# Kernel tuning notes

Measured on AMD Instinct MI355X. Metric: run time of the kernel, lower is better.

## Reference

```python
import jax, jax.numpy as jnp
import numpy as np

N_NODES = 100000
N_EDGES = 3200000
D_IN = 256
D_HID = 256
N_CLASS = 40


def setup_inputs() -> dict:
    key = jax.random.key(0)
    ks = jax.random.split(key, 8)
    x = jax.random.normal(ks[0], (N_NODES, D_IN), dtype=jnp.float32)
    edge_index = jax.random.randint(ks[1], (2, N_EDGES), 0, N_NODES, dtype=jnp.int64)
    s1 = 1.0 / np.sqrt(D_IN)
    s2 = 1.0 / np.sqrt(D_HID)
    W1_l = jax.random.normal(ks[2], (D_IN, D_HID), dtype=jnp.float32) * s1
    W1_r = jax.random.normal(ks[3], (D_IN, D_HID), dtype=jnp.float32) * s1
    b1 = jnp.zeros((D_HID,), dtype=jnp.float32)
    W2_l = jax.random.normal(ks[4], (D_HID, N_CLASS), dtype=jnp.float32) * s2
    W2_r = jax.random.normal(ks[5], (D_HID, N_CLASS), dtype=jnp.float32) * s2
    b2 = jnp.zeros((N_CLASS,), dtype=jnp.float32)
    return {"x": x, "edge_index": edge_index, "W1_l": W1_l, "W1_r": W1_r,
            "b1": b1, "W2_l": W2_l, "W2_r": W2_r, "b2": b2}


def _sage_conv(h, src, dst, deg_inv, Wl, Wr, b):
    # mean-aggregate source features into targets, then linear transforms
    agg = jax.ops.segment_sum(h[src], dst, num_segments=N_NODES)  # [N, d]
    agg = agg * deg_inv[:, None]
    return agg @ Wl + h @ Wr + b


def reference(x, edge_index, W1_l, W1_r, b1, W2_l, W2_r, b2):
    src, dst = edge_index[0], edge_index[1]
    deg = jax.ops.segment_sum(jnp.ones((src.shape[0],), dtype=x.dtype), dst,
                              num_segments=N_NODES)
    deg_inv = 1.0 / jnp.maximum(deg, 1.0)
    h = jax.nn.relu(_sage_conv(x, src, dst, deg_inv, W1_l, W1_r, b1))
    out = _sage_conv(h, src, dst, deg_inv, W2_l, W2_r, b2)
    return jax.nn.log_softmax(out, axis=1)
```

## Files before the change

kernel.cpp:

```cpp
#include <hip/hip_runtime.h>
#include <hip/hip_bf16.h>

#define THREADS 256
#define NB_MAX 400
#define NPH 13

typedef __attribute__((ext_vector_type(8))) short bf16x8;
typedef __attribute__((ext_vector_type(4))) float f32x4;
typedef __attribute__((ext_vector_type(2))) float f32x2;

__device__ __forceinline__ unsigned short f2b(float f) {
    __hip_bfloat16 h = __float2bfloat16(f);
    return *reinterpret_cast<unsigned short*>(&h);
}
__device__ __forceinline__ unsigned char f2q(float v) {
    int q = __builtin_amdgcn_cvt_pk_fp8_f32(v, v, 0, false);
    return (unsigned char)(q & 0xff);
}
__device__ __forceinline__ void gload_lds16(const void* g, void* l) {
    __builtin_amdgcn_global_load_lds(
        (const __attribute__((address_space(1))) void*)g,
        (__attribute__((address_space(3))) void*)l, 16, 0, 0);
}

__global__ __launch_bounds__(256) void k_hist(const int* __restrict__ dst, int E, int nbk,
                                              int* __restrict__ gcnt) {
    __shared__ int lc[NB_MAX];
    const int tid = threadIdx.x;
    for (int i = tid; i < nbk; i += 256) lc[i] = 0;
    __syncthreads();
    const int stride = gridDim.x * 256;
    for (int e = blockIdx.x * 256 + tid; e < E; e += stride)
        atomicAdd(&lc[dst[e] >> 8], 1);
    __syncthreads();
    for (int i = tid; i < nbk; i += 256)
        if (lc[i]) atomicAdd(&gcnt[i], lc[i]);
}

__global__ __launch_bounds__(512) void k_scanb(const int* __restrict__ gcnt, int* __restrict__ bptr,
                                               int* __restrict__ gcur, int nbk, int E) {
    __shared__ int sm[512];
    const int t = threadIdx.x;
    int v = (t < nbk) ? gcnt[t] : 0;
    sm[t] = v; __syncthreads();
    for (int off = 1; off < 512; off <<= 1) {
        int u = (t >= off) ? sm[t - off] : 0; __syncthreads();
        sm[t] += u; __syncthreads();
    }
    if (t < nbk) {
        int ex = sm[t] - v;
        bptr[t] = ex;
        gcur[t] = ex;
    }
    if (t == 0) bptr[nbk] = E;
}

__global__ __launch_bounds__(256) void k_bucket_scatter(const int* __restrict__ src, const int* __restrict__ dst,
                                                        int* __restrict__ gcur, unsigned* __restrict__ pairs,
                                                        int E, int nbk) {
    __shared__ int cnt[NB_MAX];
    __shared__ int base[NB_MAX];
    const int tid = threadIdx.x;
    const int e0 = blockIdx.x * 8192;
    for (int i = tid; i < nbk; i += 256) cnt[i] = 0;
    __syncthreads();
    #pragma unroll
    for (int j = 0; j < 32; ++j) {
        int e = e0 + j * 256 + tid;
        if (e < E) atomicAdd(&cnt[dst[e] >> 8], 1);
    }
    __syncthreads();
    for (int i = tid; i < nbk; i += 256)
        base[i] = cnt[i] ? atomicAdd(&gcur[i], cnt[i]) : 0;
    __syncthreads();
    #pragma unroll
    for (int j = 0; j < 32; ++j) {
        int e = e0 + j * 256 + tid;
        if (e < E) {
            int d = dst[e];
            int p = atomicAdd(&base[d >> 8], 1);
            pairs[p] = ((unsigned)src[e] << 8) | ((unsigned)d & 255u);
        }
    }
}

__global__ __launch_bounds__(256) void k_bucket_csr(const int* __restrict__ bptr, const unsigned* __restrict__ pairs,
                                                    int* __restrict__ rowptr, float* __restrict__ dinv,
                                                    int* __restrict__ csr_src, int N, int nbk, int E) {
    __shared__ int pc[256 * NPH];
    __shared__ int deg[256];
    __shared__ int sm[256];
    __shared__ int nodebase[256];
    const int b = blockIdx.x;
    const int tid = threadIdx.x;
    const int e0 = bptr[b], e1 = bptr[b + 1];

    #pragma unroll
    for (int i = 0; i < NPH; ++i) pc[i * 256 + tid] = 0;
    __syncthreads();
    for (int e = e0 + tid; e < e1; e += 256) {
        unsigned u = pairs[e];
        int n = (int)(u & 255u);
        int ph = (int)(u >> 8) >> 13;
        atomicAdd(&pc[ph * 256 + n], 1);
    }
    __syncthreads();
    int run = 0;
    #pragma unroll
    for (int ph = 0; ph < NPH; ++ph) {
        int c = pc[ph * 256 + tid];
        pc[ph * 256 + tid] = run;
        run += c;
    }
    int d = run;
    deg[tid] = d;
    sm[tid] = d; __syncthreads();
    for (int off = 1; off < 256; off <<= 1) {
        int u = (tid >= off) ? sm[tid - off] : 0; __syncthreads();
        sm[tid] += u; __syncthreads();
    }
    int ex = sm[tid] - d;
    int node = (b << 8) + tid;
    int nb_ = e0 + ex;
    nodebase[tid] = nb_;
    if (node < N) {
        rowptr[node] = nb_;
        dinv[node] = 1.0f / (float)max(d, 1);
    }
    if (b == nbk - 1 && tid == 0) rowptr[N] = E;
    __syncthreads();
    #pragma unroll
    for (int ph = 0; ph < NPH; ++ph) pc[ph * 256 + tid] += nodebase[tid];
    __syncthreads();
    for (int e = e0 + tid; e < e1; e += 256) {
        unsigned u = pairs[e];
        int n = (int)(u & 255u);
        int s = (int)(u >> 8);
        int p = atomicAdd(&pc[(s >> 13) * 256 + n], 1);
        csr_src[p] = s;
    }
}

__global__ __launch_bounds__(256) void k_cvt(const float* __restrict__ x, unsigned short* __restrict__ xb,
                                             unsigned char* __restrict__ xq, int N, int Npad,
                                             const float* __restrict__ W1l, const float* __restrict__ W1r,
                                             const float* __restrict__ W2l, const float* __restrict__ W2r,
                                             unsigned short* __restrict__ WbT, unsigned short* __restrict__ WbT2) {
    int i = blockIdx.x * THREADS + threadIdx.x;
    const int nxu = Npad * 32;
    if (i < nxu) {
        int row = i >> 5;
        unsigned short o[8];
        int q0 = 0, q1 = 0;
        if (row < N) {
            float4 v0 = reinterpret_cast<const float4*>(x)[2 * (size_t)i];
            float4 v1 = reinterpret_cast<const float4*>(x)[2 * (size_t)i + 1];
            o[0] = f2b(v0.x); o[1] = f2b(v0.y); o[2] = f2b(v0.z); o[3] = f2b(v0.w);
            o[4] = f2b(v1.x); o[5] = f2b(v1.y); o[6] = f2b(v1.z); o[7] = f2b(v1.w);
            q0 = __builtin_amdgcn_cvt_pk_fp8_f32(v0.x, v0.y, q0, false);
            q0 = __builtin_amdgcn_cvt_pk_fp8_f32(v0.z, v0.w, q0, true);
            q1 = __builtin_amdgcn_cvt_pk_fp8_f32(v1.x, v1.y, q1, false);
            q1 = __builtin_amdgcn_cvt_pk_fp8_f32(v1.z, v1.w, q1, true);
        } else {
            #pragma unroll
            for (int j = 0; j < 8; ++j) o[j] = 0;
        }
        reinterpret_cast<uint4*>(xb)[i] = *reinterpret_cast<uint4*>(o);
        reinterpret_cast<uint2*>(xq)[i] = make_uint2((unsigned)q0, (unsigned)q1);
        return;
    }
    int idx = i - nxu;
    if (idx < 131072) {
        int n = idx >> 9, k = idx & 511;
        float v = (k < 256) ? W1l[(size_t)k * 256 + n] : W1r[(size_t)(k - 256) * 256 + n];
        WbT[idx] = f2b(v);
    } else if (idx < 131072 + 20480) {
        int j = idx - 131072;
        int n = j >> 8, k = j & 255;
        float v = (n < 40) ? W2l[(size_t)k * 40 + n] : W2r[(size_t)k * 40 + (n - 40)];
        WbT2[j] = f2b(v);
    }
}

__global__ __launch_bounds__(256) void k_agg1(const int* __restrict__ rowptr, const int* __restrict__ csr_src,
                                              const float* __restrict__ dinv, const unsigned char* __restrict__ xq,
                                              unsigned short* __restrict__ aggb, int N, int Npad) {
    int gid = blockIdx.x * THREADS + threadIdx.x;
    int node = gid >> 5, lane = gid & 31;
    if (node >= N) {
        if (node < Npad)
            reinterpret_cast<uint4*>(aggb + (size_t)node * 256 + lane * 8)[0] = make_uint4(0, 0, 0, 0);
        return;
    }
    const int e0 = rowptr[node], e1 = rowptr[node + 1];
    const unsigned char* xl = xq + (size_t)lane * 8;
    f32x2 acc[4];
    #pragma unroll
    for (int j = 0; j < 4; ++j) acc[j] = (f32x2){0.f, 0.f};
    for (int eb = e0; eb < e1; eb += 32) {
        int n = min(32, e1 - eb);
        int sidx = (eb + lane < e1) ? csr_src[eb + lane] : 0;
        int j = 0;
        for (; j + 7 < n; j += 8) {
            uint2 vv[8];
            #pragma unroll
            for (int q = 0; q < 8; ++q) {
                int s = __shfl(sidx, j + q, 32);
                vv[q] = *reinterpret_cast<const uint2*>(xl + (size_t)s * 256);
            }
            #pragma unroll
            for (int q = 0; q < 8; ++q) {
                acc[0] += __builtin_amdgcn_cvt_pk_f32_fp8((int)vv[q].x, false);
                acc[1] += __builtin_amdgcn_cvt_pk_f32_fp8((int)vv[q].x, true);
                acc[2] += __builtin_amdgcn_cvt_pk_f32_fp8((int)vv[q].y, false);
                acc[3] += __builtin_amdgcn_cvt_pk_f32_fp8((int)vv[q].y, true);
            }
        }
        for (; j < n; ++j) {
            int s = __shfl(sidx, j, 32);
            uint2 v = *reinterpret_cast<const uint2*>(xl + (size_t)s * 256);
            acc[0] += __builtin_amdgcn_cvt_pk_f32_fp8((int)v.x, false);
            acc[1] += __builtin_amdgcn_cvt_pk_f32_fp8((int)v.x, true);
            acc[2] += __builtin_amdgcn_cvt_pk_f32_fp8((int)v.y, false);
            acc[3] += __builtin_amdgcn_cvt_pk_f32_fp8((int)v.y, true);
        }
    }
    const float ds = dinv[node];
    unsigned short o[8];
    #pragma unroll
    for (int j = 0; j < 4; ++j) {
        o[2 * j + 0] = f2b(acc[j].x * ds);
        o[2 * j + 1] = f2b(acc[j].y * ds);
    }
    *reinterpret_cast<uint4*>(aggb + (size_t)node * 256 + lane * 8) = *reinterpret_cast<uint4*>(o);
}

__global__ __launch_bounds__(512) void k_gemm1(
    const unsigned short* __restrict__ aggb, const unsigned short* __restrict__ xb,
    const unsigned short* __restrict__ WbT, const float* __restrict__ b1,
    unsigned short* __restrict__ hb, int M)
{
    __shared__ unsigned short As[128 * 64];
    __shared__ unsigned short Bs[256 * 64];

    const int tid  = threadIdx.x;
    const int lane = tid & 63;
    const int wave = tid >> 6;
    const int row0 = blockIdx.x * 128;
    const int wm0  = (wave >> 2) * 64;
    const int wn0  = (wave & 3) * 64;

    const int ldr = lane >> 3;
    const int lsw = ((lane & 7) ^ ldr) * 8;

    f32x4 acc[4][4];
    #pragma unroll
    for (int m = 0; m < 4; ++m)
        #pragma unroll
        for (int n = 0; n < 4; ++n)
            acc[m][n] = (f32x4){0.f, 0.f, 0.f, 0.f};

    for (int kt = 0; kt < 8; ++kt) {
        const unsigned short* Abase = (kt < 4) ? aggb : xb;
        const int kcol = (kt & 3) * 64;
        __syncthreads();
        #pragma unroll
        for (int i = 0; i < 2; ++i) {
            const int c = wave * 2 + i;
            const unsigned short* ga = Abase + (size_t)(row0 + c * 8 + ldr) * 256 + kcol + lsw;
            gload_lds16(ga, &As[c * 512]);
        }
        #pragma unroll
        for (int i = 0; i < 4; ++i) {
            const int c = wave * 4 + i;
            const unsigned short* gb = WbT + (size_t)(c * 8 + ldr) * 512 + kt * 64 + lsw;
            gload_lds16(gb, &Bs[c * 512]);
        }
        __syncthreads();
        #pragma unroll
        for (int kk = 0; kk < 2; ++kk) {
            bf16x8 af[4], bf[4];
            #pragma unroll
            for (int m = 0; m < 4; ++m) {
                const int r = wm0 + m * 16 + (lane & 15);
                const int s = (kk * 4 + (lane >> 4)) ^ (r & 7);
                af[m] = *reinterpret_cast<const bf16x8*>(&As[r * 64 + s * 8]);
            }
            #pragma unroll
            for (int n = 0; n < 4; ++n) {
                const int r = wn0 + n * 16 + (lane & 15);
                const int s = (kk * 4 + (lane >> 4)) ^ (r & 7);
                bf[n] = *reinterpret_cast<const bf16x8*>(&Bs[r * 64 + s * 8]);
            }
            #pragma unroll
            for (int m = 0; m < 4; ++m)
                #pragma unroll
                for (int n = 0; n < 4; ++n)
                    acc[m][n] = __builtin_amdgcn_mfma_f32_16x16x32_bf16(af[m], bf[n], acc[m][n], 0, 0, 0);
        }
    }

    const int crow = (lane >> 4) * 4;
    const int ccol = lane & 15;
    #pragma unroll
    for (int n = 0; n < 4; ++n) {
        const int col = wn0 + n * 16 + ccol;
        const float bias = b1[col];
        #pragma unroll
        for (int m = 0; m < 4; ++m) {
            const int rbase = row0 + wm0 + m * 16 + crow;
            #pragma unroll
            for (int r = 0; r < 4; ++r) {
                const int row = rbase + r;
                if (row < M) {
                    float v = fmaxf(acc[m][n][r] + bias, 0.f);
                    hb[(size_t)row * 256 + col] = f2b(v);
                }
            }
        }
    }
}

__global__ __launch_bounds__(256) void k_gemm2(
    const unsigned short* __restrict__ hb, const unsigned short* __restrict__ WbT2,
    const float* __restrict__ b2,
    unsigned char* __restrict__ Tq, float* __restrict__ Up, int M)
{
    __shared__ unsigned short As[128 * 64];
    __shared__ unsigned short Bs2[80 * 264];

    const int tid  = threadIdx.x;
    const int lane = tid & 63;
    const int wave = tid >> 6;
    const int row0 = blockIdx.x * 128;

    const int ldr = lane >> 3;
    const int lsw = ((lane & 7) ^ ldr) * 8;

    for (int idx = tid; idx < 80 * 32; idx += 256) {
        int row = idx >> 5, un = idx & 31;
        uint4 d = *reinterpret_cast<const uint4*>(WbT2 + (size_t)row * 256 + un * 8);
        *reinterpret_cast<uint4*>(&Bs2[row * 264 + un * 8]) = d;
    }

    f32x4 acc[2][5];
    #pragma unroll
    for (int m = 0; m < 2; ++m)
        #pragma unroll
        for (int n = 0; n < 5; ++n)
            acc[m][n] = (f32x4){0.f, 0.f, 0.f, 0.f};

    for (int kt = 0; kt < 4; ++kt) {
        __syncthreads();
        #pragma unroll
        for (int i = 0; i < 4; ++i) {
            const int c = wave * 4 + i;
            const unsigned short* ga = hb + (size_t)(row0 + c * 8 + ldr) * 256 + kt * 64 + lsw;
            gload_lds16(ga, &As[c * 512]);
        }
        __syncthreads();
        #pragma unroll
        for (int kk = 0; kk < 2; ++kk) {
            bf16x8 af[2], bf[5];
            #pragma unroll
            for (int m = 0; m < 2; ++m) {
                const int r = wave * 32 + m * 16 + (lane & 15);
                const int s = (kk * 4 + (lane >> 4)) ^ (r & 7);
                af[m] = *reinterpret_cast<const bf16x8*>(&As[(r & 127) * 64 + s * 8]);
            }
            #pragma unroll
            for (int n = 0; n < 5; ++n) {
                const int r = n * 16 + (lane & 15);
                bf[n] = *reinterpret_cast<const bf16x8*>(&Bs2[r * 264 + kt * 64 + kk * 32 + (lane >> 4) * 8]);
            }
            #pragma unroll
            for (int m = 0; m < 2; ++m)
                #pragma unroll
                for (int n = 0; n < 5; ++n)
                    acc[m][n] = __builtin_amdgcn_mfma_f32_16x16x32_bf16(af[m], bf[n], acc[m][n], 0, 0, 0);
        }
    }

    const int crow = (lane >> 4) * 4;
    const int ccol = lane & 15;
    #pragma unroll
    for (int n = 0; n < 5; ++n) {
        const int col = n * 16 + ccol;
        #pragma unroll
        for (int m = 0; m < 2; ++m) {
            const int rbase = row0 + wave * 32 + m * 16 + crow;
            #pragma unroll
            for (int r = 0; r < 4; ++r) {
                const int row = rbase + r;
                if (row < M) {
                    float v = acc[m][n][r];
                    if (col < 40)
                        Tq[(size_t)row * 40 + col] = f2q(v);
                    else
                        Up[(size_t)row * 40 + (col - 40)] = v + b2[col - 40];
                }
            }
        }
    }
}

__global__ __launch_bounds__(256) void k_final(const int* __restrict__ rowptr, const int* __restrict__ csr_src,
                                               const float* __restrict__ dinv, const unsigned char* __restrict__ Tq,
                                               const float* __restrict__ Up, float* __restrict__ out, int N) {
    int gid = blockIdx.x * THREADS + threadIdx.x;
    int node = gid >> 6, lane = gid & 63;
    if (node >= N) return;
    const int e0 = rowptr[node], e1 = rowptr[node + 1];
    const int g = lane / 10;
    const int c = lane % 10;
    float a0 = 0.f, a1 = 0.f, a2 = 0.f, a3 = 0.f;
    for (int eb = e0; eb < e1; eb += 64) {
        int sidx = (eb + lane < e1) ? csr_src[eb + lane] : 0;
        int nn = min(64, e1 - eb);
        for (int jb = 0; jb < nn; jb += 6) {
            int ei = jb + g;
            bool valid = (g < 6) && (ei < nn);
            int s = __shfl(sidx, ei & 63, 64);
            if (valid) {
                unsigned u = *reinterpret_cast<const unsigned*>(Tq + (size_t)s * 40 + c * 4);
                f32x2 lo = __builtin_amdgcn_cvt_pk_f32_fp8((int)u, false);
                f32x2 hi = __builtin_amdgcn_cvt_pk_f32_fp8((int)u, true);
                a0 += lo.x; a1 += lo.y;
                a2 += hi.x; a3 += hi.y;
            }
        }
    }
    float t0 = a0, t1 = a1, t2 = a2, t3 = a3;
    #pragma unroll
    for (int gg = 1; gg < 6; ++gg) {
        t0 += __shfl(a0, c + 10 * gg, 64);
        t1 += __shfl(a1, c + 10 * gg, 64);
        t2 += __shfl(a2, c + 10 * gg, 64);
        t3 += __shfl(a3, c + 10 * gg, 64);
    }
    float v0 = -1e30f, v1 = -1e30f, v2 = -1e30f, v3 = -1e30f;
    if (lane < 10) {
        const float ds = dinv[node];
        float4 up = *reinterpret_cast<const float4*>(Up + (size_t)node * 40 + lane * 4);
        v0 = t0 * ds + up.x; v1 = t1 * ds + up.y;
        v2 = t2 * ds + up.z; v3 = t3 * ds + up.w;
    }
    float m = fmaxf(fmaxf(v0, v1), fmaxf(v2, v3));
    #pragma unroll
    for (int o = 8; o > 0; o >>= 1) m = fmaxf(m, __shfl_xor(m, o, 16));
    float e = 0.f;
    if (lane < 10) e = expf(v0 - m) + expf(v1 - m) + expf(v2 - m) + expf(v3 - m);
    float ssum = e;
    #pragma unroll
    for (int o = 8; o > 0; o >>= 1) ssum += __shfl_xor(ssum, o, 16);
    float ls = logf(ssum);
    if (lane < 10) {
        float4 o4;
        o4.x = v0 - m - ls; o4.y = v1 - m - ls;
        o4.z = v2 - m - ls; o4.w = v3 - m - ls;
        *reinterpret_cast<float4*>(out + (size_t)node * 40 + lane * 4) = o4;
    }
}

extern "C" void kernel_launch(void* const* d_in, const int* in_sizes, int n_in,
                              void* d_out, int out_size, void* d_ws, size_t ws_size,
                              hipStream_t stream) {
    const float* x   = (const float*)d_in[0];
    const int*   ei  = (const int*)d_in[1];
    const float* W1l = (const float*)d_in[2];
    const float* W1r = (const float*)d_in[3];
    const float* b1  = (const float*)d_in[4];
    const float* W2l = (const float*)d_in[5];
    const float* W2r = (const float*)d_in[6];
    const float* b2  = (const float*)d_in[7];
    float* out = (float*)d_out;

    const int N = in_sizes[0] / 256;
    const int E = in_sizes[1] / 2;
    const int Npad = ((N + 127) / 128) * 128;
    const int nbk = (N + 255) / 256;
    const int* src = ei;
    const int* dst = ei + E;

    char* ws = (char*)d_ws;
    size_t off = 0;
    int*   gcnt    = (int*)(ws + off); off += (size_t)NB_MAX * 4;
    int*   bptr    = (int*)(ws + off); off += (size_t)(NB_MAX + 1) * 4;
    int*   gcur    = (int*)(ws + off); off += (size_t)NB_MAX * 4;
    int*   rowptr  = (int*)(ws + off); off += (size_t)(N + 1) * 4;
    float* dinv    = (float*)(ws + off); off += (size_t)N * 4;
    off = (off + 255) & ~(size_t)255;
    unsigned* pairs = (unsigned*)(ws + off); off += (size_t)E * 4;
    int*   csr_src = (int*)(ws + off); off += (size_t)E * 4;
    off = (off + 255) & ~(size_t)255;
    unsigned short* xb   = (unsigned short*)(ws + off); off += (size_t)Npad * 256 * 2;
    unsigned char*  xq   = (unsigned char*)(ws + off);  off += (size_t)Npad * 256;
    unsigned short* aggb = (unsigned short*)(ws + off); off += (size_t)Npad * 256 * 2;
    unsigned short* hb   = (unsigned short*)(ws + off); off += (size_t)Npad * 256 * 2;
    unsigned short* WbT  = (unsigned short*)(ws + off); off += (size_t)256 * 512 * 2;
    unsigned short* WbT2 = (unsigned short*)(ws + off); off += (size_t)80 * 256 * 2;
    off = (off + 255) & ~(size_t)255;
    unsigned char*  Tq   = (unsigned char*)(ws + off);  off += (size_t)Npad * 40;
    off = (off + 255) & ~(size_t)255;
    float*          Up   = (float*)(ws + off);          off += (size_t)Npad * 40 * 4;

    hipMemsetAsync(gcnt, 0, (size_t)NB_MAX * 4, stream);

    const int nsb = (E + 8191) / 8192;
    k_hist<<<nsb, THREADS, 0, stream>>>(dst, E, nbk, gcnt);
    k_scanb<<<1, 512, 0, stream>>>(gcnt, bptr, gcur, nbk, E);
    k_bucket_scatter<<<nsb, THREADS, 0, stream>>>(src, dst, gcur, pairs, E, nbk);
    k_bucket_csr<<<nbk, THREADS, 0, stream>>>(bptr, pairs, rowptr, dinv, csr_src, N, nbk, E);

    const int ncvt = Npad * 32 + 131072 + 20480;
    k_cvt<<<(ncvt + THREADS - 1) / THREADS, THREADS, 0, stream>>>(x, xb, xq, N, Npad,
                                                                  W1l, W1r, W2l, W2r, WbT, WbT2);

    k_agg1<<<((size_t)Npad * 32 + THREADS - 1) / THREADS, THREADS, 0, stream>>>(rowptr, csr_src, dinv, xq, aggb, N, Npad);

    k_gemm1<<<Npad / 128, 512, 0, stream>>>(aggb, xb, WbT, b1, hb, N);

    k_gemm2<<<Npad / 128, THREADS, 0, stream>>>(hb, WbT2, b2, Tq, Up, N);

    k_final<<<((size_t)N * 64 + THREADS - 1) / THREADS, THREADS, 0, stream>>>(rowptr, csr_src, dinv, Tq, Up, out, N);
}
```

Measured before the change: 401.4 us.

## Phase-synchronized aggregation over source-range phases and fuse histogram with conversion

The first-layer aggregation now runs as a persistent grid. Each half-wave owns 13 nodes and walks the 13 source-ID phases in lockstep, with a block barrier between phases. The aim is for all blocks to gather from the same slice of the fp8 feature table at once, so that slice stays in L2. The CSR build also writes per-phase row pointers, and the edge histogram is merged with the feature and weight conversion into one launch. In exchange the kernel holds 13 accumulator sets in registers, which may spill or cut occupancy, the 8-wide unrolled gather loop is dropped, and load balance across nodes gets worse.

```diff
diff --git a/kernel.cpp b/kernel.cpp
--- a/kernel.cpp
+++ b/kernel.cpp
@@ -4,6 +4,8 @@
 #define THREADS 256
 #define NB_MAX 400
 #define NPH 13
+#define NB_AGG 1024
+#define OWN 13
 
 typedef __attribute__((ext_vector_type(8))) short bf16x8;
 typedef __attribute__((ext_vector_type(4))) float f32x4;
@@ -23,130 +25,27 @@
         (__attribute__((address_space(3))) void*)l, 16, 0, 0);
 }
 
-__global__ __launch_bounds__(256) void k_hist(const int* __restrict__ dst, int E, int nbk,
-                                              int* __restrict__ gcnt) {
+__global__ __launch_bounds__(256) void k_hist_cvt(
+    const int* __restrict__ dst, int E, int nbk, int* __restrict__ gcnt, int nsb,
+    const float* __restrict__ x, unsigned short* __restrict__ xb, unsigned char* __restrict__ xq,
+    int N, int Npad,
+    const float* __restrict__ W1l, const float* __restrict__ W1r,
+    const float* __restrict__ W2l, const float* __restrict__ W2r,
+    unsigned short* __restrict__ WbT, unsigned short* __restrict__ WbT2) {
     __shared__ int lc[NB_MAX];
     const int tid = threadIdx.x;
-    for (int i = tid; i < nbk; i += 256) lc[i] = 0;
-    __syncthreads();
-    const int stride = gridDim.x * 256;
-    for (int e = blockIdx.x * 256 + tid; e < E; e += stride)
-        atomicAdd(&lc[dst[e] >> 8], 1);
-    __syncthreads();
-    for (int i = tid; i < nbk; i += 256)
-        if (lc[i]) atomicAdd(&gcnt[i], lc[i]);
-}
-
-__global__ __launch_bounds__(512) void k_scanb(const int* __restrict__ gcnt, int* __restrict__ bptr,
-                                               int* __restrict__ gcur, int nbk, int E) {
-    __shared__ int sm[512];
-    const int t = threadIdx.x;
-    int v = (t < nbk) ? gcnt[t] : 0;
-    sm[t] = v; __syncthreads();
-    for (int off = 1; off < 512; off <<= 1) {
-        int u = (t >= off) ? sm[t - off] : 0; __syncthreads();
-        sm[t] += u; __syncthreads();
-    }
-    if (t < nbk) {
-        int ex = sm[t] - v;
-        bptr[t] = ex;
-        gcur[t] = ex;
-    }
-    if (t == 0) bptr[nbk] = E;
-}
-
-__global__ __launch_bounds__(256) void k_bucket_scatter(const int* __restrict__ src, const int* __restrict__ dst,
-                                                        int* __restrict__ gcur, unsigned* __restrict__ pairs,
-                                                        int E, int nbk) {
-    __shared__ int cnt[NB_MAX];
-    __shared__ int base[NB_MAX];
-    const int tid = threadIdx.x;
-    const int e0 = blockIdx.x * 8192;
-    for (int i = tid; i < nbk; i += 256) cnt[i] = 0;
-    __syncthreads();
-    #pragma unroll
-    for (int j = 0; j < 32; ++j) {
-        int e = e0 + j * 256 + tid;
-        if (e < E) atomicAdd(&cnt[dst[e] >> 8], 1);
-    }
-    __syncthreads();
-    for (int i = tid; i < nbk; i += 256)
-        base[i] = cnt[i] ? atomicAdd(&gcur[i], cnt[i]) : 0;
-    __syncthreads();
-    #pragma unroll
-    for (int j = 0; j < 32; ++j) {
-        int e = e0 + j * 256 + tid;
-        if (e < E) {
-            int d = dst[e];
-            int p = atomicAdd(&base[d >> 8], 1);
-            pairs[p] = ((unsigned)src[e] << 8) | ((unsigned)d & 255u);
-        }
-    }
-}
-
-__global__ __launch_bounds__(256) void k_bucket_csr(const int* __restrict__ bptr, const unsigned* __restrict__ pairs,
-                                                    int* __restrict__ rowptr, float* __restrict__ dinv,
-                                                    int* __restrict__ csr_src, int N, int nbk, int E) {
-    __shared__ int pc[256 * NPH];
-    __shared__ int deg[256];
-    __shared__ int sm[256];
-    __shared__ int nodebase[256];
-    const int b = blockIdx.x;
-    const int tid = threadIdx.x;
-    const int e0 = bptr[b], e1 = bptr[b + 1];
-
-    #pragma unroll
-    for (int i = 0; i < NPH; ++i) pc[i * 256 + tid] = 0;
-    __syncthreads();
-    for (int e = e0 + tid; e < e1; e += 256) {
-        unsigned u = pairs[e];
-        int n = (int)(u & 255u);
-        int ph = (int)(u >> 8) >> 13;
-        atomicAdd(&pc[ph * 256 + n], 1);
-    }
-    __syncthreads();
-    int run = 0;
-    #pragma unroll
-    for (int ph = 0; ph < NPH; ++ph) {
-        int c = pc[ph * 256 + tid];
-        pc[ph * 256 + tid] = run;
-        run += c;
-    }
-    int d = run;
-    deg[tid] = d;
-    sm[tid] = d; __syncthreads();
-    for (int off = 1; off < 256; off <<= 1) {
-        int u = (tid >= off) ? sm[tid - off] : 0; __syncthreads();
-        sm[tid] += u; __syncthreads();
-    }
-    int ex = sm[tid] - d;
-    int node = (b << 8) + tid;
-    int nb_ = e0 + ex;
-    nodebase[tid] = nb_;
-    if (node < N) {
-        rowptr[node] = nb_;
-        dinv[node] = 1.0f / (float)max(d, 1);
-    }
-    if (b == nbk - 1 && tid == 0) rowptr[N] = E;
-    __syncthreads();
-    #pragma unroll
-    for (int ph = 0; ph < NPH; ++ph) pc[ph * 256 + tid] += nodebase[tid];
-    __syncthreads();
-    for (int e = e0 + tid; e < e1; e += 256) {
-        unsigned u = pairs[e];
-        int n = (int)(u & 255u);
-        int s = (int)(u >> 8);
-        int p = atomicAdd(&pc[(s >> 13) * 256 + n], 1);
-        csr_src[p] = s;
-    }
-}
-
-__global__ __launch_bounds__(256) void k_cvt(const float* __restrict__ x, unsigned short* __restrict__ xb,
-                                             unsigned char* __restrict__ xq, int N, int Npad,
-                                             const float* __restrict__ W1l, const float* __restrict__ W1r,
-                                             const float* __restrict__ W2l, const float* __restrict__ W2r,
-                                             unsigned short* __restrict__ WbT, unsigned short* __restrict__ WbT2) {
-    int i = blockIdx.x * THREADS + threadIdx.x;
+    if ((int)blockIdx.x < nsb) {
+        for (int i = tid; i < nbk; i += 256) lc[i] = 0;
+        __syncthreads();
+        const int stride = nsb * 256;
+        for (int e = blockIdx.x * 256 + tid; e < E; e += stride)
+            atomicAdd(&lc[dst[e] >> 8], 1);
+        __syncthreads();
+        for (int i = tid; i < nbk; i += 256)
+            if (lc[i]) atomicAdd(&gcnt[i], lc[i]);
+        return;
+    }
+    int i = ((int)blockIdx.x - nsb) * 256 + tid;
     const int nxu = Npad * 32;
     if (i < nxu) {
         int row = i >> 5;
@@ -182,57 +81,169 @@
     }
 }
 
-__global__ __launch_bounds__(256) void k_agg1(const int* __restrict__ rowptr, const int* __restrict__ csr_src,
+__global__ __launch_bounds__(512) void k_scanb(const int* __restrict__ gcnt, int* __restrict__ bptr,
+                                               int* __restrict__ gcur, int nbk, int E) {
+    __shared__ int sm[512];
+    const int t = threadIdx.x;
+    int v = (t < nbk) ? gcnt[t] : 0;
+    sm[t] = v; __syncthreads();
+    for (int off = 1; off < 512; off <<= 1) {
+        int u = (t >= off) ? sm[t - off] : 0; __syncthreads();
+        sm[t] += u; __syncthreads();
+    }
+    if (t < nbk) {
+        int ex = sm[t] - v;
+        bptr[t] = ex;
+        gcur[t] = ex;
+    }
+    if (t == 0) bptr[nbk] = E;
+}
+
+__global__ __launch_bounds__(256) void k_bucket_scatter(const int* __restrict__ src, const int* __restrict__ dst,
+                                                        int* __restrict__ gcur, unsigned* __restrict__ pairs,
+                                                        int E, int nbk) {
+    __shared__ int cnt[NB_MAX];
+    __shared__ int base[NB_MAX];
+    const int tid = threadIdx.x;
+    const int e0 = blockIdx.x * 8192;
+    for (int i = tid; i < nbk; i += 256) cnt[i] = 0;
+    __syncthreads();
+    #pragma unroll
+    for (int j = 0; j < 32; ++j) {
+        int e = e0 + j * 256 + tid;
+        if (e < E) atomicAdd(&cnt[dst[e] >> 8], 1);
+    }
+    __syncthreads();
+    for (int i = tid; i < nbk; i += 256)
+        base[i] = cnt[i] ? atomicAdd(&gcur[i], cnt[i]) : 0;
+    __syncthreads();
+    #pragma unroll
+    for (int j = 0; j < 32; ++j) {
+        int e = e0 + j * 256 + tid;
+        if (e < E) {
+            int d = dst[e];
+            int p = atomicAdd(&base[d >> 8], 1);
+            pairs[p] = ((unsigned)src[e] << 8) | ((unsigned)d & 255u);
+        }
+    }
+}
+
+__global__ __launch_bounds__(256) void k_bucket_csr(const int* __restrict__ bptr, const unsigned* __restrict__ pairs,
+                                                    int* __restrict__ rowptr, int* __restrict__ rowptr2,
+                                                    float* __restrict__ dinv,
+                                                    int* __restrict__ csr_src, int N, int nbk, int E) {
+    __shared__ int pc[256 * NPH];
+    __shared__ int deg[256];
+    __shared__ int sm[256];
+    __shared__ int nodebase[256];
+    const int b = blockIdx.x;
+    const int tid = threadIdx.x;
+    const int e0 = bptr[b], e1 = bptr[b + 1];
+
+    #pragma unroll
+    for (int i = 0; i < NPH; ++i) pc[i * 256 + tid] = 0;
+    __syncthreads();
+    for (int e = e0 + tid; e < e1; e += 256) {
+        unsigned u = pairs[e];
+        int n = (int)(u & 255u);
+        int ph = (int)(u >> 8) >> 13;
+        atomicAdd(&pc[ph * 256 + n], 1);
+    }
+    __syncthreads();
+    int run = 0;
+    #pragma unroll
+    for (int ph = 0; ph < NPH; ++ph) {
+        int c = pc[ph * 256 + tid];
+        pc[ph * 256 + tid] = run;
+        run += c;
+    }
+    int d = run;
+    deg[tid] = d;
+    sm[tid] = d; __syncthreads();
+    for (int off = 1; off < 256; off <<= 1) {
+        int u = (tid >= off) ? sm[tid - off] : 0; __syncthreads();
+        sm[tid] += u; __syncthreads();
+    }
+    int ex = sm[tid] - d;
+    int node = (b << 8) + tid;
+    int nb_ = e0 + ex;
+    nodebase[tid] = nb_;
+    if (node < N) {
+        rowptr[node] = nb_;
+        dinv[node] = 1.0f / (float)max(d, 1);
+    }
+    if (b == nbk - 1 && tid == 0) rowptr[N] = E;
+    __syncthreads();
+    #pragma unroll
+    for (int ph = 0; ph < NPH; ++ph) {
+        int cu = pc[ph * 256 + tid] + nodebase[tid];
+        pc[ph * 256 + tid] = cu;
+        if (node < N) rowptr2[(size_t)ph * N + node] = cu;
+    }
+    if (node < N) rowptr2[(size_t)NPH * N + node] = nb_ + d;
+    __syncthreads();
+    for (int e = e0 + tid; e < e1; e += 256) {
+        unsigned u = pairs[e];
+        int n = (int)(u & 255u);
+        int s = (int)(u >> 8);
+        int p = atomicAdd(&pc[(s >> 13) * 256 + n], 1);
+        csr_src[p] = s;
+    }
+}
+
+__global__ __launch_bounds__(256) void k_agg1(const int* __restrict__ rowptr2, const int* __restrict__ csr_src,
                                               const float* __restrict__ dinv, const unsigned char* __restrict__ xq,
-                                              unsigned short* __restrict__ aggb, int N, int Npad) {
-    int gid = blockIdx.x * THREADS + threadIdx.x;
-    int node = gid >> 5, lane = gid & 31;
-    if (node >= N) {
-        if (node < Npad)
-            reinterpret_cast<uint4*>(aggb + (size_t)node * 256 + lane * 8)[0] = make_uint4(0, 0, 0, 0);
-        return;
-    }
-    const int e0 = rowptr[node], e1 = rowptr[node + 1];
+                                              unsigned short* __restrict__ aggb, int N, int Npad, int H) {
+    const int tid = threadIdx.x;
+    const int hw = blockIdx.x * 8 + (tid >> 5);
+    const int lane = tid & 31;
     const unsigned char* xl = xq + (size_t)lane * 8;
-    f32x2 acc[4];
-    #pragma unroll
-    for (int j = 0; j < 4; ++j) acc[j] = (f32x2){0.f, 0.f};
-    for (int eb = e0; eb < e1; eb += 32) {
-        int n = min(32, e1 - eb);
-        int sidx = (eb + lane < e1) ? csr_src[eb + lane] : 0;
-        int j = 0;
-        for (; j + 7 < n; j += 8) {
-            uint2 vv[8];
-            #pragma unroll
-            for (int q = 0; q < 8; ++q) {
-                int s = __shfl(sidx, j + q, 32);
-                vv[q] = *reinterpret_cast<const uint2*>(xl + (size_t)s * 256);
-            }
-            #pragma unroll
-            for (int q = 0; q < 8; ++q) {
-                acc[0] += __builtin_amdgcn_cvt_pk_f32_fp8((int)vv[q].x, false);
-                acc[1] += __builtin_amdgcn_cvt_pk_f32_fp8((int)vv[q].x, true);
-                acc[2] += __builtin_amdgcn_cvt_pk_f32_fp8((int)vv[q].y, false);
-                acc[3] += __builtin_amdgcn_cvt_pk_f32_fp8((int)vv[q].y, true);
-            }
-        }
-        for (; j < n; ++j) {
-            int s = __shfl(sidx, j, 32);
-            uint2 v = *reinterpret_cast<const uint2*>(xl + (size_t)s * 256);
-            acc[0] += __builtin_amdgcn_cvt_pk_f32_fp8((int)v.x, false);
-            acc[1] += __builtin_amdgcn_cvt_pk_f32_fp8((int)v.x, true);
-            acc[2] += __builtin_amdgcn_cvt_pk_f32_fp8((int)v.y, false);
-            acc[3] += __builtin_amdgcn_cvt_pk_f32_fp8((int)v.y, true);
-        }
-    }
-    const float ds = dinv[node];
-    unsigned short o[8];
-    #pragma unroll
-    for (int j = 0; j < 4; ++j) {
-        o[2 * j + 0] = f2b(acc[j].x * ds);
-        o[2 * j + 1] = f2b(acc[j].y * ds);
-    }
-    *reinterpret_cast<uint4*>(aggb + (size_t)node * 256 + lane * 8) = *reinterpret_cast<uint4*>(o);
+
+    f32x2 acc[OWN][4];
+    #pragma unroll
+    for (int i = 0; i < OWN; ++i)
+        #pragma unroll
+        for (int j = 0; j < 4; ++j) acc[i][j] = (f32x2){0.f, 0.f};
+
+    for (int ph = 0; ph < NPH; ++ph) {
+        #pragma unroll
+        for (int i = 0; i < OWN; ++i) {
+            const int node = hw + i * H;
+            if (node >= N) continue;
+            const int s0 = rowptr2[(size_t)ph * N + node];
+            const int s1 = rowptr2[(size_t)(ph + 1) * N + node];
+            for (int eb = s0; eb < s1; eb += 32) {
+                int cnt = min(32, s1 - eb);
+                int sidx = (eb + lane < s1) ? csr_src[eb + lane] : 0;
+                for (int j = 0; j < cnt; ++j) {
+                    int s = __shfl(sidx, j, 32);
+                    uint2 v = *reinterpret_cast<const uint2*>(xl + (size_t)s * 256);
+                    acc[i][0] += __builtin_amdgcn_cvt_pk_f32_fp8((int)v.x, false);
+                    acc[i][1] += __builtin_amdgcn_cvt_pk_f32_fp8((int)v.x, true);
+                    acc[i][2] += __builtin_amdgcn_cvt_pk_f32_fp8((int)v.y, false);
+                    acc[i][3] += __builtin_amdgcn_cvt_pk_f32_fp8((int)v.y, true);
+                }
+            }
+        }
+        __syncthreads();
+    }
+
+    #pragma unroll
+    for (int i = 0; i < OWN; ++i) {
+        const int node = hw + i * H;
+        if (node < N) {
+            const float ds = dinv[node];
+            unsigned short o[8];
+            #pragma unroll
+            for (int j = 0; j < 4; ++j) {
+                o[2 * j + 0] = f2b(acc[i][j].x * ds);
+                o[2 * j + 1] = f2b(acc[i][j].y * ds);
+            }
+            *reinterpret_cast<uint4*>(aggb + (size_t)node * 256 + lane * 8) = *reinterpret_cast<uint4*>(o);
+        } else if (node < Npad) {
+            *reinterpret_cast<uint4*>(aggb + (size_t)node * 256 + lane * 8) = make_uint4(0, 0, 0, 0);
+        }
+    }
 }
 
 __global__ __launch_bounds__(512) void k_gemm1(
@@ -490,6 +501,8 @@
     int*   rowptr  = (int*)(ws + off); off += (size_t)(N + 1) * 4;
     float* dinv    = (float*)(ws + off); off += (size_t)N * 4;
     off = (off + 255) & ~(size_t)255;
+    int*   rowptr2 = (int*)(ws + off); off += (size_t)(NPH + 1) * N * 4;
+    off = (off + 255) & ~(size_t)255;
     unsigned* pairs = (unsigned*)(ws + off); off += (size_t)E * 4;
     int*   csr_src = (int*)(ws + off); off += (size_t)E * 4;
     off = (off + 255) & ~(size_t)255;
@@ -507,16 +520,16 @@
     hipMemsetAsync(gcnt, 0, (size_t)NB_MAX * 4, stream);
 
     const int nsb = (E + 8191) / 8192;
-    k_hist<<<nsb, THREADS, 0, stream>>>(dst, E, nbk, gcnt);
+    const int ncvt_blocks = (Npad * 32 + 131072 + 20480 + THREADS - 1) / THREADS;
+    k_hist_cvt<<<nsb + ncvt_blocks, THREADS, 0, stream>>>(dst, E, nbk, gcnt, nsb,
+                                                          x, xb, xq, N, Npad,
+                                                          W1l, W1r, W2l, W2r, WbT, WbT2);
     k_scanb<<<1, 512, 0, stream>>>(gcnt, bptr, gcur, nbk, E);
     k_bucket_scatter<<<nsb, THREADS, 0, stream>>>(src, dst, gcur, pairs, E, nbk);
-    k_bucket_csr<<<nbk, THREADS, 0, stream>>>(bptr, pairs, rowptr, dinv, csr_src, N, nbk, E);
-
-    const int ncvt = Npad * 32 + 131072 + 20480;
-    k_cvt<<<(ncvt + THREADS - 1) / THREADS, THREADS, 0, stream>>>(x, xb, xq, N, Npad,
-                                                                  W1l, W1r, W2l, W2r, WbT, WbT2);
-
-    k_agg1<<<((size_t)Npad * 32 + THREADS - 1) / THREADS, THREADS, 0, stream>>>(rowptr, csr_src, dinv, xq, aggb, N, Npad);
+    k_bucket_csr<<<nbk, THREADS, 0, stream>>>(bptr, pairs, rowptr, rowptr2, dinv, csr_src, N, nbk, E);
+
+    const int H = NB_AGG * 8;
+    k_agg1<<<NB_AGG, THREADS, 0, stream>>>(rowptr2, csr_src, dinv, xq, aggb, N, Npad, H);
 
     k_gemm1<<<Npad / 128, 512, 0, stream>>>(aggb, xb, WbT, b1, hb, N);
 
```

Measured after the change: 848.0 us. 111% more time.

## Fuse histogram with conversion kernel and pad FP8 logits rows to 64 bytes

Applied to the files above, without the earlier changes.

The edge-destination histogram and the x/weight conversion now run as one launch, with blocks split by index, so the conversion overlaps the histogram and one launch is saved. The FP8 layer-2 projection buffer is padded from 40 to 64 bytes per row with zeroed padding. This lets the final gather kernel have 8 lanes read 8 bytes each per edge, processing 8 edges per step instead of 6 with a tree reduction. The trade-off is more gather bytes per edge plus extra padding writes in gemm2.

```diff
diff --git a/kernel.cpp b/kernel.cpp
--- a/kernel.cpp
+++ b/kernel.cpp
@@ -23,130 +23,27 @@
         (__attribute__((address_space(3))) void*)l, 16, 0, 0);
 }
 
-__global__ __launch_bounds__(256) void k_hist(const int* __restrict__ dst, int E, int nbk,
-                                              int* __restrict__ gcnt) {
+__global__ __launch_bounds__(256) void k_hist_cvt(
+    const int* __restrict__ dst, int E, int nbk, int* __restrict__ gcnt, int nsb,
+    const float* __restrict__ x, unsigned short* __restrict__ xb, unsigned char* __restrict__ xq,
+    int N, int Npad,
+    const float* __restrict__ W1l, const float* __restrict__ W1r,
+    const float* __restrict__ W2l, const float* __restrict__ W2r,
+    unsigned short* __restrict__ WbT, unsigned short* __restrict__ WbT2) {
     __shared__ int lc[NB_MAX];
     const int tid = threadIdx.x;
-    for (int i = tid; i < nbk; i += 256) lc[i] = 0;
-    __syncthreads();
-    const int stride = gridDim.x * 256;
-    for (int e = blockIdx.x * 256 + tid; e < E; e += stride)
-        atomicAdd(&lc[dst[e] >> 8], 1);
-    __syncthreads();
-    for (int i = tid; i < nbk; i += 256)
-        if (lc[i]) atomicAdd(&gcnt[i], lc[i]);
-}
-
-__global__ __launch_bounds__(512) void k_scanb(const int* __restrict__ gcnt, int* __restrict__ bptr,
-                                               int* __restrict__ gcur, int nbk, int E) {
-    __shared__ int sm[512];
-    const int t = threadIdx.x;
-    int v = (t < nbk) ? gcnt[t] : 0;
-    sm[t] = v; __syncthreads();
-    for (int off = 1; off < 512; off <<= 1) {
-        int u = (t >= off) ? sm[t - off] : 0; __syncthreads();
-        sm[t] += u; __syncthreads();
-    }
-    if (t < nbk) {
-        int ex = sm[t] - v;
-        bptr[t] = ex;
-        gcur[t] = ex;
-    }
-    if (t == 0) bptr[nbk] = E;
-}
-
-__global__ __launch_bounds__(256) void k_bucket_scatter(const int* __restrict__ src, const int* __restrict__ dst,
-                                                        int* __restrict__ gcur, unsigned* __restrict__ pairs,
-                                                        int E, int nbk) {
-    __shared__ int cnt[NB_MAX];
-    __shared__ int base[NB_MAX];
-    const int tid = threadIdx.x;
-    const int e0 = blockIdx.x * 8192;
-    for (int i = tid; i < nbk; i += 256) cnt[i] = 0;
-    __syncthreads();
-    #pragma unroll
-    for (int j = 0; j < 32; ++j) {
-        int e = e0 + j * 256 + tid;
-        if (e < E) atomicAdd(&cnt[dst[e] >> 8], 1);
-    }
-    __syncthreads();
-    for (int i = tid; i < nbk; i += 256)
-        base[i] = cnt[i] ? atomicAdd(&gcur[i], cnt[i]) : 0;
-    __syncthreads();
-    #pragma unroll
-    for (int j = 0; j < 32; ++j) {
-        int e = e0 + j * 256 + tid;
-        if (e < E) {
-            int d = dst[e];
-            int p = atomicAdd(&base[d >> 8], 1);
-            pairs[p] = ((unsigned)src[e] << 8) | ((unsigned)d & 255u);
-        }
-    }
-}
-
-__global__ __launch_bounds__(256) void k_bucket_csr(const int* __restrict__ bptr, const unsigned* __restrict__ pairs,
-                                                    int* __restrict__ rowptr, float* __restrict__ dinv,
-                                                    int* __restrict__ csr_src, int N, int nbk, int E) {
-    __shared__ int pc[256 * NPH];
-    __shared__ int deg[256];
-    __shared__ int sm[256];
-    __shared__ int nodebase[256];
-    const int b = blockIdx.x;
-    const int tid = threadIdx.x;
-    const int e0 = bptr[b], e1 = bptr[b + 1];
-
-    #pragma unroll
-    for (int i = 0; i < NPH; ++i) pc[i * 256 + tid] = 0;
-    __syncthreads();
-    for (int e = e0 + tid; e < e1; e += 256) {
-        unsigned u = pairs[e];
-        int n = (int)(u & 255u);
-        int ph = (int)(u >> 8) >> 13;
-        atomicAdd(&pc[ph * 256 + n], 1);
-    }
-    __syncthreads();
-    int run = 0;
-    #pragma unroll
-    for (int ph = 0; ph < NPH; ++ph) {
-        int c = pc[ph * 256 + tid];
-        pc[ph * 256 + tid] = run;
-        run += c;
-    }
-    int d = run;
-    deg[tid] = d;
-    sm[tid] = d; __syncthreads();
-    for (int off = 1; off < 256; off <<= 1) {
-        int u = (tid >= off) ? sm[tid - off] : 0; __syncthreads();
-        sm[tid] += u; __syncthreads();
-    }
-    int ex = sm[tid] - d;
-    int node = (b << 8) + tid;
-    int nb_ = e0 + ex;
-    nodebase[tid] = nb_;
-    if (node < N) {
-        rowptr[node] = nb_;
-        dinv[node] = 1.0f / (float)max(d, 1);
-    }
-    if (b == nbk - 1 && tid == 0) rowptr[N] = E;
-    __syncthreads();
-    #pragma unroll
-    for (int ph = 0; ph < NPH; ++ph) pc[ph * 256 + tid] += nodebase[tid];
-    __syncthreads();
-    for (int e = e0 + tid; e < e1; e += 256) {
-        unsigned u = pairs[e];
-        int n = (int)(u & 255u);
-        int s = (int)(u >> 8);
-        int p = atomicAdd(&pc[(s >> 13) * 256 + n], 1);
-        csr_src[p] = s;
-    }
-}
-
-__global__ __launch_bounds__(256) void k_cvt(const float* __restrict__ x, unsigned short* __restrict__ xb,
-                                             unsigned char* __restrict__ xq, int N, int Npad,
-                                             const float* __restrict__ W1l, const float* __restrict__ W1r,
-                                             const float* __restrict__ W2l, const float* __restrict__ W2r,
-                                             unsigned short* __restrict__ WbT, unsigned short* __restrict__ WbT2) {
-    int i = blockIdx.x * THREADS + threadIdx.x;
+    if ((int)blockIdx.x < nsb) {
+        for (int i = tid; i < nbk; i += 256) lc[i] = 0;
+        __syncthreads();
+        const int stride = nsb * 256;
+        for (int e = blockIdx.x * 256 + tid; e < E; e += stride)
+            atomicAdd(&lc[dst[e] >> 8], 1);
+        __syncthreads();
+        for (int i = tid; i < nbk; i += 256)
+            if (lc[i]) atomicAdd(&gcnt[i], lc[i]);
+        return;
+    }
+    int i = ((int)blockIdx.x - nsb) * 256 + tid;
     const int nxu = Npad * 32;
     if (i < nxu) {
         int row = i >> 5;
@@ -182,6 +79,108 @@
     }
 }
 
+__global__ __launch_bounds__(512) void k_scanb(const int* __restrict__ gcnt, int* __restrict__ bptr,
+                                               int* __restrict__ gcur, int nbk, int E) {
+    __shared__ int sm[512];
+    const int t = threadIdx.x;
+    int v = (t < nbk) ? gcnt[t] : 0;
+    sm[t] = v; __syncthreads();
+    for (int off = 1; off < 512; off <<= 1) {
+        int u = (t >= off) ? sm[t - off] : 0; __syncthreads();
+        sm[t] += u; __syncthreads();
+    }
+    if (t < nbk) {
+        int ex = sm[t] - v;
+        bptr[t] = ex;
+        gcur[t] = ex;
+    }
+    if (t == 0) bptr[nbk] = E;
+}
+
+__global__ __launch_bounds__(256) void k_bucket_scatter(const int* __restrict__ src, const int* __restrict__ dst,
+                                                        int* __restrict__ gcur, unsigned* __restrict__ pairs,
+                                                        int E, int nbk) {
+    __shared__ int cnt[NB_MAX];
+    __shared__ int base[NB_MAX];
+    const int tid = threadIdx.x;
+    const int e0 = blockIdx.x * 8192;
+    for (int i = tid; i < nbk; i += 256) cnt[i] = 0;
+    __syncthreads();
+    #pragma unroll
+    for (int j = 0; j < 32; ++j) {
+        int e = e0 + j * 256 + tid;
+        if (e < E) atomicAdd(&cnt[dst[e] >> 8], 1);
+    }
+    __syncthreads();
+    for (int i = tid; i < nbk; i += 256)
+        base[i] = cnt[i] ? atomicAdd(&gcur[i], cnt[i]) : 0;
+    __syncthreads();
+    #pragma unroll
+    for (int j = 0; j < 32; ++j) {
+        int e = e0 + j * 256 + tid;
+        if (e < E) {
+            int d = dst[e];
+            int p = atomicAdd(&base[d >> 8], 1);
+            pairs[p] = ((unsigned)src[e] << 8) | ((unsigned)d & 255u);
+        }
+    }
+}
+
+__global__ __launch_bounds__(256) void k_bucket_csr(const int* __restrict__ bptr, const unsigned* __restrict__ pairs,
+                                                    int* __restrict__ rowptr, float* __restrict__ dinv,
+                                                    int* __restrict__ csr_src, int N, int nbk, int E) {
+    __shared__ int pc[256 * NPH];
+    __shared__ int sm[256];
+    __shared__ int nodebase[256];
+    const int b = blockIdx.x;
+    const int tid = threadIdx.x;
+    const int e0 = bptr[b], e1 = bptr[b + 1];
+
+    #pragma unroll
+    for (int i = 0; i < NPH; ++i) pc[i * 256 + tid] = 0;
+    __syncthreads();
+    for (int e = e0 + tid; e < e1; e += 256) {
+        unsigned u = pairs[e];
+        int n = (int)(u & 255u);
+        int ph = (int)(u >> 8) >> 13;
+        atomicAdd(&pc[ph * 256 + n], 1);
+    }
+    __syncthreads();
+    int run = 0;
+    #pragma unroll
+    for (int ph = 0; ph < NPH; ++ph) {
+        int c = pc[ph * 256 + tid];
+        pc[ph * 256 + tid] = run;
+        run += c;
+    }
+    int d = run;
+    sm[tid] = d; __syncthreads();
+    for (int off = 1; off < 256; off <<= 1) {
+        int u = (tid >= off) ? sm[tid - off] : 0; __syncthreads();
+        sm[tid] += u; __syncthreads();
+    }
+    int ex = sm[tid] - d;
+    int node = (b << 8) + tid;
+    int nb_ = e0 + ex;
+    nodebase[tid] = nb_;
+    if (node < N) {
+        rowptr[node] = nb_;
+        dinv[node] = 1.0f / (float)max(d, 1);
+    }
+    if (b == nbk - 1 && tid == 0) rowptr[N] = E;
+    __syncthreads();
+    #pragma unroll
+    for (int ph = 0; ph < NPH; ++ph) pc[ph * 256 + tid] += nodebase[tid];
+    __syncthreads();
+    for (int e = e0 + tid; e < e1; e += 256) {
+        unsigned u = pairs[e];
+        int n = (int)(u & 255u);
+        int s = (int)(u >> 8);
+        int p = atomicAdd(&pc[(s >> 13) * 256 + n], 1);
+        csr_src[p] = s;
+    }
+}
+
 __global__ __launch_bounds__(256) void k_agg1(const int* __restrict__ rowptr, const int* __restrict__ csr_src,
                                               const float* __restrict__ dinv, const unsigned char* __restrict__ xq,
                                               unsigned short* __restrict__ aggb, int N, int Npad) {
@@ -395,12 +394,17 @@
                 if (row < M) {
                     float v = acc[m][n][r];
                     if (col < 40)
-                        Tq[(size_t)row * 40 + col] = f2q(v);
+                        Tq[(size_t)row * 64 + col] = f2q(v);
                     else
                         Up[(size_t)row * 40 + (col - 40)] = v + b2[col - 40];
                 }
             }
         }
+    }
+    for (int i = tid; i < 128 * 24; i += 256) {
+        int r = i / 24, c = 40 + (i % 24);
+        int row = row0 + r;
+        if (row < M) Tq[(size_t)row * 64 + c] = 0;
     }
 }
 
@@ -411,54 +415,64 @@
     int node = gid >> 6, lane = gid & 63;
     if (node >= N) return;
     const int e0 = rowptr[node], e1 = rowptr[node + 1];
-    const int g = lane / 10;
-    const int c = lane % 10;
-    float a0 = 0.f, a1 = 0.f, a2 = 0.f, a3 = 0.f;
+    const int c8 = lane & 7;
+    const int e5 = lane >> 3;
+    f32x2 acc[4];
+    #pragma unroll
+    for (int i = 0; i < 4; ++i) acc[i] = (f32x2){0.f, 0.f};
     for (int eb = e0; eb < e1; eb += 64) {
         int sidx = (eb + lane < e1) ? csr_src[eb + lane] : 0;
         int nn = min(64, e1 - eb);
-        for (int jb = 0; jb < nn; jb += 6) {
-            int ei = jb + g;
-            bool valid = (g < 6) && (ei < nn);
+        for (int jb = 0; jb < nn; jb += 8) {
+            int ei = jb + e5;
             int s = __shfl(sidx, ei & 63, 64);
-            if (valid) {
-                unsigned u = *reinterpret_cast<const unsigned*>(Tq + (size_t)s * 40 + c * 4);
-                f32x2 lo = __builtin_amdgcn_cvt_pk_f32_fp8((int)u, false);
-                f32x2 hi = __builtin_amdgcn_cvt_pk_f32_fp8((int)u, true);
-                a0 += lo.x; a1 += lo.y;
-                a2 += hi.x; a3 += hi.y;
-            }
-        }
-    }
-    float t0 = a0, t1 = a1, t2 = a2, t3 = a3;
-    #pragma unroll
-    for (int gg = 1; gg < 6; ++gg) {
-        t0 += __shfl(a0, c + 10 * gg, 64);
-        t1 += __shfl(a1, c + 10 * gg, 64);
-        t2 += __shfl(a2, c + 10 * gg, 64);
-        t3 += __shfl(a3, c + 10 * gg, 64);
-    }
-    float v0 = -1e30f, v1 = -1e30f, v2 = -1e30f, v3 = -1e30f;
-    if (lane < 10) {
+            if (ei < nn) {
+                uint2 u = *reinterpret_cast<const uint2*>(Tq + (size_t)s * 64 + c8 * 8);
+                acc[0] += __builtin_amdgcn_cvt_pk_f32_fp8((int)u.x, false);
+                acc[1] += __builtin_amdgcn_cvt_pk_f32_fp8((int)u.x, true);
+                acc[2] += __builtin_amdgcn_cvt_pk_f32_fp8((int)u.y, false);
+                acc[3] += __builtin_amdgcn_cvt_pk_f32_fp8((int)u.y, true);
+            }
+        }
+    }
+    #pragma unroll
+    for (int st = 8; st <= 32; st <<= 1) {
+        #pragma unroll
+        for (int i = 0; i < 4; ++i) {
+            acc[i].x += __shfl_xor(acc[i].x, st, 64);
+            acc[i].y += __shfl_xor(acc[i].y, st, 64);
+        }
+    }
+    const bool act = (e5 == 0) && (c8 < 5);
+    float v[8];
+    float m = -1e30f;
+    if (act) {
         const float ds = dinv[node];
-        float4 up = *reinterpret_cast<const float4*>(Up + (size_t)node * 40 + lane * 4);
-        v0 = t0 * ds + up.x; v1 = t1 * ds + up.y;
-        v2 = t2 * ds + up.z; v3 = t3 * ds + up.w;
-    }
-    float m = fmaxf(fmaxf(v0, v1), fmaxf(v2, v3));
-    #pragma unroll
-    for (int o = 8; o > 0; o >>= 1) m = fmaxf(m, __shfl_xor(m, o, 16));
+        float4 ua = *reinterpret_cast<const float4*>(Up + (size_t)node * 40 + c8 * 8);
+        float4 ub = *reinterpret_cast<const float4*>(Up + (size_t)node * 40 + c8 * 8 + 4);
+        v[0] = acc[0].x * ds + ua.x; v[1] = acc[0].y * ds + ua.y;
+        v[2] = acc[1].x * ds + ua.z; v[3] = acc[1].y * ds + ua.w;
+        v[4] = acc[2].x * ds + ub.x; v[5] = acc[2].y * ds + ub.y;
+        v[6] = acc[3].x * ds + ub.z; v[7] = acc[3].y * ds + ub.w;
+        #pragma unroll
+        for (int i = 0; i < 8; ++i) m = fmaxf(m, v[i]);
+    }
+    #pragma unroll
+    for (int o = 4; o > 0; o >>= 1) m = fmaxf(m, __shfl_xor(m, o, 8));
     float e = 0.f;
-    if (lane < 10) e = expf(v0 - m) + expf(v1 - m) + expf(v2 - m) + expf(v3 - m);
-    float ssum = e;
-    #pragma unroll
-    for (int o = 8; o > 0; o >>= 1) ssum += __shfl_xor(ssum, o, 16);
-    float ls = logf(ssum);
-    if (lane < 10) {
-        float4 o4;
-        o4.x = v0 - m - ls; o4.y = v1 - m - ls;
-        o4.z = v2 - m - ls; o4.w = v3 - m - ls;
-        *reinterpret_cast<float4*>(out + (size_t)node * 40 + lane * 4) = o4;
+    if (act) {
+        #pragma unroll
+        for (int i = 0; i < 8; ++i) e += expf(v[i] - m);
+    }
+    #pragma unroll
+    for (int o = 4; o > 0; o >>= 1) e += __shfl_xor(e, o, 8);
+    float ls = logf(e);
+    if (act) {
+        float4 oa, ob;
+        oa.x = v[0] - m - ls; oa.y = v[1] - m - ls; oa.z = v[2] - m - ls; oa.w = v[3] - m - ls;
+        ob.x = v[4] - m - ls; ob.y = v[5] - m - ls; ob.z = v[6] - m - ls; ob.w = v[7] - m - ls;
+        *reinterpret_cast<float4*>(out + (size_t)node * 40 + c8 * 8) = oa;
+        *reinterpret_cast<float4*>(out + (size_t)node * 40 + c8 * 8 + 4) = ob;
     }
 }
 
@@ -500,22 +514,21 @@
     unsigned short* WbT  = (unsigned short*)(ws + off); off += (size_t)256 * 512 * 2;
     unsigned short* WbT2 = (unsigned short*)(ws + off); off += (size_t)80 * 256 * 2;
     off = (off + 255) & ~(size_t)255;
-    unsigned char*  Tq   = (unsigned char*)(ws + off);  off += (size_t)Npad * 40;
+    unsigned char*  Tq   = (unsigned char*)(ws + off);  off += (size_t)Npad * 64;
     off = (off + 255) & ~(size_t)255;
     float*          Up   = (float*)(ws + off);          off += (size_t)Npad * 40 * 4;
 
     hipMemsetAsync(gcnt, 0, (size_t)NB_MAX * 4, stream);
 
     const int nsb = (E + 8191) / 8192;
-    k_hist<<<nsb, THREADS, 0, stream>>>(dst, E, nbk, gcnt);
+    const int ncvt_blocks = (Npad * 32 + 131072 + 20480 + THREADS - 1) / THREADS;
+    k_hist_cvt<<<nsb + ncvt_blocks, THREADS, 0, stream>>>(dst, E, nbk, gcnt, nsb,
+                                                          x, xb, xq, N, Npad,
+                                                          W1l, W1r, W2l, W2r, WbT, WbT2);
     k_scanb<<<1, 512, 0, stream>>>(gcnt, bptr, gcur, nbk, E);
     k_bucket_scatter<<<nsb, THREADS, 0, stream>>>(src, dst, gcur, pairs, E, nbk);
     k_bucket_csr<<<nbk, THREADS, 0, stream>>>(bptr, pairs, rowptr, dinv, csr_src, N, nbk, E);
 
-    const int ncvt = Npad * 32 + 131072 + 20480;
-    k_cvt<<<(ncvt + THREADS - 1) / THREADS, THREADS, 0, stream>>>(x, xb, xq, N, Npad,
-                                                                  W1l, W1r, W2l, W2r, WbT, WbT2);
-
     k_agg1<<<((size_t)Npad * 32 + THREADS - 1) / THREADS, THREADS, 0, stream>>>(rowptr, csr_src, dinv, xq, aggb, N, Npad);
 
     k_gemm1<<<Npad / 128, 512, 0, stream>>>(aggb, xb, WbT, b1, hb, N);
```

Result: no change. 399.8 us (-0.4%).
